# Optimization experiments

Hardware: AMD Instinct MI355X
Metric: run time of the kernel (lower is better)

The kernel has to match this reference:

```python
import jax, jax.numpy as jnp
import numpy as np

IN_DIM = 256
OUT_DIM = 64   # per-head dim
NUM_HEADS = 8
B = 8
N = 1024


def setup_inputs() -> dict:
    key = jax.random.key(0)
    k_adj, k_h, kq, kk, kv, kbq, kbk, kbv = jax.random.split(key, 8)
    adj_matrix = jax.random.randint(k_adj, (N, N), 0, 2, dtype=jnp.int32)
    h = jax.random.normal(k_h, (B, N, IN_DIM), dtype=jnp.float32)
    s = 1.0 / np.sqrt(IN_DIM)
    Wq = jax.random.normal(kq, (IN_DIM, OUT_DIM * NUM_HEADS), dtype=jnp.float32) * s
    Wk = jax.random.normal(kk, (IN_DIM, OUT_DIM * NUM_HEADS), dtype=jnp.float32) * s
    Wv = jax.random.normal(kv, (IN_DIM, OUT_DIM * NUM_HEADS), dtype=jnp.float32) * s
    bq = jax.random.normal(kbq, (OUT_DIM * NUM_HEADS,), dtype=jnp.float32) * 0.01
    bk = jax.random.normal(kbk, (OUT_DIM * NUM_HEADS,), dtype=jnp.float32) * 0.01
    bv = jax.random.normal(kbv, (OUT_DIM * NUM_HEADS,), dtype=jnp.float32) * 0.01
    return {"adj_matrix": adj_matrix, "h": h, "Wq": Wq, "bq": bq,
            "Wk": Wk, "bk": bk, "Wv": Wv, "bv": bv}


def reference(adj_matrix, h, Wq, bq, Wk, bk, Wv, bv):
    B_, N_, _ = h.shape
    H, D = NUM_HEADS, OUT_DIM
    Qh = (h @ Wq + bq).reshape(B_, N_, H, D)
    Kh = (h @ Wk + bk).reshape(B_, N_, H, D)
    Vh = (h @ Wv + bv).reshape(B_, N_, H, D)
    scores = jnp.einsum('bnhd,bmhd->bhnm', Qh, Kh) / jnp.sqrt(jnp.float32(D))
    # adjacency mask broadcast over batch and heads (neigh_attention=True)
    scores = jnp.where(adj_matrix[None, None, :, :] == 0, -jnp.inf, scores)
    attn = jax.nn.softmax(scores, axis=-1)
    out = jnp.einsum('bhnm,bmhd->bnhd', attn, Vh)
    return out.reshape(B_, N_, H * D)
```

## Files before the change

kernel.cpp:

```cpp
#include <hip/hip_runtime.h>
#include <hip/hip_bf16.h>
#include <math.h>

#define IN_DIM 256
#define HD     512
#define NHEADS 8
#define DH     64
#define NSEQ   1024
#define BATCH  8

#define QSCALE 0.18033688011112042f

typedef unsigned short u16;
typedef unsigned int   u32;
typedef short bf16x8 __attribute__((ext_vector_type(8)));
typedef float f32x4  __attribute__((ext_vector_type(4)));

#if __has_builtin(__builtin_amdgcn_exp2f)
#define EXP2(x) __builtin_amdgcn_exp2f(x)
#else
#define EXP2(x) __expf(0.69314718056f * (x))
#endif

static __device__ __forceinline__ u16 f2bf(float x) {
    u32 u = __builtin_bit_cast(u32, x);
    u += 0x7FFFu + ((u >> 16) & 1u);
    return (u16)(u >> 16);
}
static __device__ __forceinline__ float bf2f(u16 x) {
    return __builtin_bit_cast(float, ((u32)x) << 16);
}
static __device__ __forceinline__ u32 pk(u16 a, u16 b) {
    return (u32)a | ((u32)b << 16);
}
static __device__ __forceinline__ u32 cvtpk(float a, float b) {
    __hip_bfloat162 t = __float22bfloat162_rn(make_float2(a, b));
    u32 r; __builtin_memcpy(&r, &t, 4);
    return r;
}

__global__ __launch_bounds__(256)
void wtrans_kernel(const float* __restrict__ Wq, const float* __restrict__ Wk,
                   const float* __restrict__ Wv, u16* __restrict__ Wt)
{
    __shared__ float tile[64 * 65];
    const int bid = blockIdx.x, tid = threadIdx.x;
    const int k0 = (bid & 3) * 64, n0 = ((bid >> 2) & 7) * 64, wsel = bid >> 5;
    const float* W = (wsel == 0) ? Wq : (wsel == 1) ? Wk : Wv;
    u16* Out = Wt + (size_t)wsel * HD * IN_DIM;

    const int r = tid >> 2, c0 = (tid & 3) * 16;
#pragma unroll
    for (int j = 0; j < 16; j += 4) {
        float4 v = *(const float4*)(W + (size_t)(k0 + r) * HD + n0 + c0 + j);
        tile[r * 65 + c0 + j + 0] = v.x; tile[r * 65 + c0 + j + 1] = v.y;
        tile[r * 65 + c0 + j + 2] = v.z; tile[r * 65 + c0 + j + 3] = v.w;
    }
    __syncthreads();
    const int n = tid >> 2, ks = (tid & 3) * 16;
    u16 o[16];
#pragma unroll
    for (int j = 0; j < 16; ++j) o[j] = f2bf(tile[(ks + j) * 65 + n]);
    uint4 u0, u1;
    u0.x = pk(o[0], o[1]);   u0.y = pk(o[2], o[3]);
    u0.z = pk(o[4], o[5]);   u0.w = pk(o[6], o[7]);
    u1.x = pk(o[8], o[9]);   u1.y = pk(o[10], o[11]);
    u1.z = pk(o[12], o[13]); u1.w = pk(o[14], o[15]);
    u16* dst = Out + (size_t)(n0 + n) * IN_DIM + k0 + ks;
    *(uint4*)(dst) = u0;
    *(uint4*)(dst + 8) = u1;
}

__global__ __launch_bounds__(256, 4)
void gemm_mask_kernel(const float* __restrict__ h, const u16* __restrict__ Wt,
                      const int* __restrict__ adj,
                      const float* __restrict__ bq, const float* __restrict__ bk,
                      const float* __restrict__ bv,
                      u16* __restrict__ Qg, u16* __restrict__ Kg,
                      u16* __restrict__ Vtg, u16* __restrict__ MaddT)
{
    __shared__ u16 pool[64 * 64 + 3 * 64 * 64];
    const int tid = threadIdx.x;

    if (blockIdx.y >= 8) {
        int* tile = (int*)pool;
        const int abid = (blockIdx.y - 8) * 128 + blockIdx.x;
        const int tR = abid >> 4, tC = abid & 15;
        const int r = tid >> 2, cg = (tid & 3) * 16;
        const int* src = adj + (size_t)(tR * 64 + r) * NSEQ + tC * 64 + cg;
#pragma unroll
        for (int j = 0; j < 16; j += 4) {
            int4 a = *(const int4*)(src + j);
            tile[r * 65 + cg + j + 0] = a.x; tile[r * 65 + cg + j + 1] = a.y;
            tile[r * 65 + cg + j + 2] = a.z; tile[r * 65 + cg + j + 3] = a.w;
        }
        __syncthreads();
        const int kk = tid >> 2, qg = (tid & 3) * 16;
        u16 o[16];
#pragma unroll
        for (int j = 0; j < 16; ++j)
            o[j] = (tile[(qg + j) * 65 + kk] == 0) ? (u16)0xFF7F : (u16)0;
        uint4 u0, u1;
        u0.x = pk(o[0], o[1]);   u0.y = pk(o[2], o[3]);
        u0.z = pk(o[4], o[5]);   u0.w = pk(o[6], o[7]);
        u1.x = pk(o[8], o[9]);   u1.y = pk(o[10], o[11]);
        u1.z = pk(o[12], o[13]); u1.w = pk(o[14], o[15]);
        u16* dst = MaddT + (size_t)(tC * 64 + kk) * NSEQ + tR * 64 + qg;
        *(uint4*)(dst) = u0;
        *(uint4*)(dst + 8) = u1;
        return;
    }

    u16* As = pool;
    u16* Bs = pool + 64 * 64;

    const int m0 = blockIdx.x * 64;
    const int hh = blockIdx.y;
    const int n0 = hh * 64;

    const int w = tid >> 6, lane = tid & 63, l15 = lane & 15, quad = lane >> 4;
    const int sw = l15 & 7;

    f32x4 acc[3][4];
#pragma unroll
    for (int wh = 0; wh < 3; ++wh)
#pragma unroll
        for (int t = 0; t < 4; ++t) acc[wh][t] = (f32x4){0.f, 0.f, 0.f, 0.f};

    const int arow = tid >> 2, acg = (tid & 3) * 2;
    const int brow = tid & 63, bgrp = tid >> 6;
    const float* srcA = h + (size_t)(m0 + arow) * IN_DIM;

    for (int kk = 0; kk < IN_DIM; kk += 64) {
        __syncthreads();
#pragma unroll
        for (int g = 0; g < 2; ++g) {
            const float* p = srcA + kk + (acg + g) * 8;
            float4 v0 = *(const float4*)(p);
            float4 v1 = *(const float4*)(p + 4);
            uint4 u;
            u.x = cvtpk(v0.x, v0.y); u.y = cvtpk(v0.z, v0.w);
            u.z = cvtpk(v1.x, v1.y); u.w = cvtpk(v1.z, v1.w);
            *(uint4*)&As[arow * 64 + (((acg + g) ^ (arow & 7)) * 8)] = u;
        }
#pragma unroll
        for (int i = 0; i < 6; ++i) {
            const int gc = bgrp * 6 + i;
            const int wh = gc >> 3, c8 = gc & 7;
            *(uint4*)&Bs[wh * 4096 + brow * 64 + ((c8 ^ (brow & 7)) * 8)] =
                *(const uint4*)(Wt + (size_t)wh * HD * IN_DIM +
                                (size_t)(n0 + brow) * IN_DIM + kk + c8 * 8);
        }
        __syncthreads();
        const int ra = (w * 16 + l15) * 64;
        bf16x8 a0 = *(const bf16x8*)&As[ra + ((quad ^ sw) * 8)];
        bf16x8 a1 = *(const bf16x8*)&As[ra + (((4 + quad) ^ sw) * 8)];
#pragma unroll
        for (int t = 0; t < 4; ++t) {
            const int rb = (t * 16 + l15) * 64;
#pragma unroll
            for (int wh = 0; wh < 3; ++wh) {
                bf16x8 b0 = *(const bf16x8*)&Bs[wh * 4096 + rb + ((quad ^ sw) * 8)];
                bf16x8 b1 = *(const bf16x8*)&Bs[wh * 4096 + rb + (((4 + quad) ^ sw) * 8)];
                acc[wh][t] = __builtin_amdgcn_mfma_f32_16x16x32_bf16(a0, b0, acc[wh][t], 0, 0, 0);
                acc[wh][t] = __builtin_amdgcn_mfma_f32_16x16x32_bf16(a1, b1, acc[wh][t], 0, 0, 0);
            }
        }
    }

    for (int which = 0; which < 2; ++which) {
        u16* T = pool;
        const float* bias = (which == 0) ? bq : bk;
        u16* Out = (which == 0) ? Qg : Kg;
        const float scale = (which == 0) ? QSCALE : 1.0f;
        __syncthreads();
#pragma unroll
        for (int t = 0; t < 4; ++t) {
            const float bvv = bias[n0 + t * 16 + l15];
            const int rowb = w * 16 + quad * 4;
#pragma unroll
            for (int r = 0; r < 4; ++r)
                T[(rowb + r) * 72 + t * 16 + l15] =
                    f2bf((acc[which][t][r] + bvv) * scale);
        }
        __syncthreads();
        const int row = tid >> 2, qc = (tid & 3) * 16;
        u16* dst = Out + (size_t)(m0 + row) * HD + n0 + qc;
        const u16* srcT = &T[row * 72 + qc];
        *(uint4*)(dst)     = *(const uint4*)(srcT);
        *(uint4*)(dst + 8) = *(const uint4*)(srcT + 8);
    }

    {
        u16* T = pool;
        __syncthreads();
#pragma unroll
        for (int t = 0; t < 4; ++t) {
            const float bvv = bv[n0 + t * 16 + l15];
            const int trow = (t * 16 + l15) * 72;
#pragma unroll
            for (int r = 0; r < 4; ++r)
                T[trow + (quad * 4 + r) * 4 + w] = f2bf(acc[2][t][r] + bvv);
        }
        __syncthreads();
        const int b = m0 >> 10, nloc = m0 & 1023;
        const int d = tid >> 2, c = (tid & 3) * 16;
        u16* dst = Vtg + ((size_t)(b * NHEADS + hh) * DH + d) * NSEQ + nloc + c;
        *(uint4*)(dst)     = *(uint4*)&T[d * 72 + c];
        *(uint4*)(dst + 8) = *(uint4*)&T[d * 72 + c + 8];
    }
}

__global__ __launch_bounds__(256, 4)
void attn_kernel(const u16* __restrict__ MaddT, const u16* __restrict__ Qg,
                 const u16* __restrict__ Kg, const u16* __restrict__ Vtg,
                 float* __restrict__ out)
{
    __shared__ u16 Ks[2][64 * 64];
    __shared__ u16 Vs[2][64 * 64];
    __shared__ u16 Ps[64 * 64];

    const int tid = threadIdx.x;
    const int w = tid >> 6, lane = tid & 63, l15 = lane & 15, quad = lane >> 4;
    const int bh = blockIdx.x, qt = blockIdx.y;
    const int b = bh >> 3;
    const int n0 = qt * 64;
    const size_t rowbase = (size_t)b * NSEQ;
    const int colbase = (bh & 7) * DH;
    const int sw = l15 & 7;

    const u16* qrow = Qg + (rowbase + n0 + w * 16 + l15) * HD + colbase;
    const bf16x8 qa0 = *(const bf16x8*)(qrow + quad * 8);
    const bf16x8 qa1 = *(const bf16x8*)(qrow + 32 + quad * 8);

    const int srow = tid >> 2, cp = (tid & 3) * 2;
    const int swc0 = ((cp ^ (srow & 7)) * 8), swc1 = (((cp + 1) ^ (srow & 7)) * 8);
    const u16* kgp = Kg + (rowbase + srow) * HD + colbase + cp * 8;
    const u16* vgp = Vtg + ((size_t)bh * DH + srow) * NSEQ + cp * 8;
    const u16* mgp = MaddT + (size_t)l15 * NSEQ + n0 + w * 16 + quad * 4;

    uint4 kG0 = *(const uint4*)kgp, kG1 = *(const uint4*)(kgp + 8);
    uint4 vG0 = *(const uint4*)vgp, vG1 = *(const uint4*)(vgp + 8);
    ushort4 mG[4];
#pragma unroll
    for (int t = 0; t < 4; ++t) mG[t] = *(const ushort4*)(mgp + (size_t)(t * 16) * NSEQ);

    *(uint4*)&Ks[0][srow * 64 + swc0] = kG0;
    *(uint4*)&Ks[0][srow * 64 + swc1] = kG1;
    *(uint4*)&Vs[0][srow * 64 + swc0] = vG0;
    *(uint4*)&Vs[0][srow * 64 + swc1] = vG1;
    __syncthreads();

    float lrow[4] = {0.f, 0.f, 0.f, 0.f};
    f32x4 O[4];
#pragma unroll
    for (int t = 0; t < 4; ++t) O[t] = (f32x4){0.f, 0.f, 0.f, 0.f};

    const int pwbase = (w * 16 + quad * 4) * 64;
    const int parow  = (w * 16 + l15) * 64;

    for (int ch = 0; ch < 16; ++ch) {
        const int cur = ch & 1;

        f32x4 s4[4];
#pragma unroll
        for (int t = 0; t < 4; ++t)
            s4[t] = (f32x4){bf2f(mG[t].x), bf2f(mG[t].y),
                            bf2f(mG[t].z), bf2f(mG[t].w)};

        if (ch < 15) {
            kG0 = *(const uint4*)(kgp + (size_t)(ch + 1) * 64 * HD);
            kG1 = *(const uint4*)(kgp + (size_t)(ch + 1) * 64 * HD + 8);
            vG0 = *(const uint4*)(vgp + (ch + 1) * 64);
            vG1 = *(const uint4*)(vgp + (ch + 1) * 64 + 8);
#pragma unroll
            for (int t = 0; t < 4; ++t)
                mG[t] = *(const ushort4*)(mgp + ((size_t)(ch + 1) * 64 + t * 16) * NSEQ);
        }

#pragma unroll
        for (int t = 0; t < 4; ++t) {
            const int rb = (t * 16 + l15) * 64;
            bf16x8 kb0 = *(const bf16x8*)&Ks[cur][rb + ((quad ^ sw) * 8)];
            bf16x8 kb1 = *(const bf16x8*)&Ks[cur][rb + (((4 + quad) ^ sw) * 8)];
            s4[t] = __builtin_amdgcn_mfma_f32_16x16x32_bf16(qa0, kb0, s4[t], 0, 0, 0);
            s4[t] = __builtin_amdgcn_mfma_f32_16x16x32_bf16(qa1, kb1, s4[t], 0, 0, 0);
        }

        if (ch < 15) {
            *(uint4*)&Ks[1 - cur][srow * 64 + swc0] = kG0;
            *(uint4*)&Ks[1 - cur][srow * 64 + swc1] = kG1;
            *(uint4*)&Vs[1 - cur][srow * 64 + swc0] = vG0;
            *(uint4*)&Vs[1 - cur][srow * 64 + swc1] = vG1;
        }

#pragma unroll
        for (int r = 0; r < 4; ++r) {
            float p0 = EXP2(s4[0][r]);
            float p1 = EXP2(s4[1][r]);
            float p2 = EXP2(s4[2][r]);
            float p3 = EXP2(s4[3][r]);
            lrow[r] += (p0 + p1) + (p2 + p3);
            uint2 pw;
            pw.x = cvtpk(p0, p1);
            pw.y = cvtpk(p2, p3);
            const int q7 = (quad * 4 + r) & 7;
            *(uint2*)&Ps[pwbase + r * 64 + (((l15 >> 1) ^ q7) * 8) + (l15 & 1) * 4] = pw;
        }

        {
            bf16x8 pa0 = *(const bf16x8*)&Ps[parow + ((quad ^ sw) * 8)];
            bf16x8 pa1 = *(const bf16x8*)&Ps[parow + (((4 + quad) ^ sw) * 8)];
#pragma unroll
            for (int t = 0; t < 4; ++t) {
                const int rb = (t * 16 + l15) * 64;
                bf16x8 vb0 = *(const bf16x8*)&Vs[cur][rb + ((quad ^ sw) * 8)];
                bf16x8 vb1 = *(const bf16x8*)&Vs[cur][rb + (((4 + quad) ^ sw) * 8)];
                O[t] = __builtin_amdgcn_mfma_f32_16x16x32_bf16(pa0, vb0, O[t], 0, 0, 0);
                O[t] = __builtin_amdgcn_mfma_f32_16x16x32_bf16(pa1, vb1, O[t], 0, 0, 0);
            }
        }
        __syncthreads();
    }

#pragma unroll
    for (int d = 1; d < 16; d <<= 1)
#pragma unroll
        for (int r = 0; r < 4; ++r)
            lrow[r] += __shfl_xor(lrow[r], d, 64);

    float inv[4];
#pragma unroll
    for (int r = 0; r < 4; ++r) inv[r] = 1.0f / lrow[r];
#pragma unroll
    for (int t = 0; t < 4; ++t)
#pragma unroll
        for (int r = 0; r < 4; ++r)
            out[(rowbase + n0 + w * 16 + quad * 4 + r) * HD + colbase + t * 16 + l15] =
                O[t][r] * inv[r];
}

extern "C" void kernel_launch(void* const* d_in, const int* in_sizes, int n_in,
                              void* d_out, int out_size, void* d_ws, size_t ws_size,
                              hipStream_t stream) {
    const int*   adj = (const int*)d_in[0];
    const float* h   = (const float*)d_in[1];
    const float* Wq  = (const float*)d_in[2];
    const float* bq  = (const float*)d_in[3];
    const float* Wk  = (const float*)d_in[4];
    const float* bk  = (const float*)d_in[5];
    const float* Wv  = (const float*)d_in[6];
    const float* bv  = (const float*)d_in[7];
    float* outp = (float*)d_out;

    u16* Wt    = (u16*)d_ws;
    u16* Qg    = Wt + (size_t)3 * HD * IN_DIM;
    u16* Kg    = Qg + (size_t)BATCH * NSEQ * HD;
    u16* Vtg   = Kg + (size_t)BATCH * NSEQ * HD;
    u16* MaddT = Vtg + (size_t)BATCH * NSEQ * HD;

    wtrans_kernel<<<96, 256, 0, stream>>>(Wq, Wk, Wv, Wt);
    gemm_mask_kernel<<<dim3(BATCH * NSEQ / 64, 10), 256, 0, stream>>>(
        h, Wt, adj, bq, bk, bv, Qg, Kg, Vtg, MaddT);
    attn_kernel<<<dim3(BATCH * NHEADS, NSEQ / 64), 256, 0, stream>>>(
        MaddT, Qg, Kg, Vtg, outp);
}
```

Measured before the change: 143.4 us.

## Enlarge attention query tile to 128 rows with 512-thread blocks

Doubles the attention block to 8 waves handling 128 query rows, so each K/V chunk staged in shared memory is reused by twice as many query rows. Each thread now loads a single 16-byte K and V vector per chunk instead of two, and the P scratch buffer is doubled. This halves the number of blocks and raises the per-block shared-memory and thread footprint, which may reduce occupancy or wave-level parallelism across the GPU.

```diff
diff --git a/kernel.cpp b/kernel.cpp
--- a/kernel.cpp
+++ b/kernel.cpp
@@ -211,20 +211,20 @@
     }
 }
 
-__global__ __launch_bounds__(256, 4)
+__global__ __launch_bounds__(512, 4)
 void attn_kernel(const u16* __restrict__ MaddT, const u16* __restrict__ Qg,
                  const u16* __restrict__ Kg, const u16* __restrict__ Vtg,
                  float* __restrict__ out)
 {
     __shared__ u16 Ks[2][64 * 64];
     __shared__ u16 Vs[2][64 * 64];
-    __shared__ u16 Ps[64 * 64];
+    __shared__ u16 Ps[128 * 64];
 
     const int tid = threadIdx.x;
     const int w = tid >> 6, lane = tid & 63, l15 = lane & 15, quad = lane >> 4;
     const int bh = blockIdx.x, qt = blockIdx.y;
     const int b = bh >> 3;
-    const int n0 = qt * 64;
+    const int n0 = qt * 128;
     const size_t rowbase = (size_t)b * NSEQ;
     const int colbase = (bh & 7) * DH;
     const int sw = l15 & 7;
@@ -233,22 +233,20 @@
     const bf16x8 qa0 = *(const bf16x8*)(qrow + quad * 8);
     const bf16x8 qa1 = *(const bf16x8*)(qrow + 32 + quad * 8);
 
-    const int srow = tid >> 2, cp = (tid & 3) * 2;
-    const int swc0 = ((cp ^ (srow & 7)) * 8), swc1 = (((cp + 1) ^ (srow & 7)) * 8);
-    const u16* kgp = Kg + (rowbase + srow) * HD + colbase + cp * 8;
-    const u16* vgp = Vtg + ((size_t)bh * DH + srow) * NSEQ + cp * 8;
+    const int srow = tid >> 3, c8w = tid & 7;
+    const int swc = ((c8w ^ (srow & 7)) * 8);
+    const u16* kgp = Kg + (rowbase + srow) * HD + colbase + c8w * 8;
+    const u16* vgp = Vtg + ((size_t)bh * DH + srow) * NSEQ + c8w * 8;
     const u16* mgp = MaddT + (size_t)l15 * NSEQ + n0 + w * 16 + quad * 4;
 
-    uint4 kG0 = *(const uint4*)kgp, kG1 = *(const uint4*)(kgp + 8);
-    uint4 vG0 = *(const uint4*)vgp, vG1 = *(const uint4*)(vgp + 8);
+    uint4 kG = *(const uint4*)kgp;
+    uint4 vG = *(const uint4*)vgp;
     ushort4 mG[4];
 #pragma unroll
     for (int t = 0; t < 4; ++t) mG[t] = *(const ushort4*)(mgp + (size_t)(t * 16) * NSEQ);
 
-    *(uint4*)&Ks[0][srow * 64 + swc0] = kG0;
-    *(uint4*)&Ks[0][srow * 64 + swc1] = kG1;
-    *(uint4*)&Vs[0][srow * 64 + swc0] = vG0;
-    *(uint4*)&Vs[0][srow * 64 + swc1] = vG1;
+    *(uint4*)&Ks[0][srow * 64 + swc] = kG;
+    *(uint4*)&Vs[0][srow * 64 + swc] = vG;
     __syncthreads();
 
     float lrow[4] = {0.f, 0.f, 0.f, 0.f};
@@ -269,10 +267,8 @@
                             bf2f(mG[t].z), bf2f(mG[t].w)};
 
         if (ch < 15) {
-            kG0 = *(const uint4*)(kgp + (size_t)(ch + 1) * 64 * HD);
-            kG1 = *(const uint4*)(kgp + (size_t)(ch + 1) * 64 * HD + 8);
-            vG0 = *(const uint4*)(vgp + (ch + 1) * 64);
-            vG1 = *(const uint4*)(vgp + (ch + 1) * 64 + 8);
+            kG = *(const uint4*)(kgp + (size_t)(ch + 1) * 64 * HD);
+            vG = *(const uint4*)(vgp + (ch + 1) * 64);
 #pragma unroll
             for (int t = 0; t < 4; ++t)
                 mG[t] = *(const ushort4*)(mgp + ((size_t)(ch + 1) * 64 + t * 16) * NSEQ);
@@ -288,10 +284,8 @@
         }
 
         if (ch < 15) {
-            *(uint4*)&Ks[1 - cur][srow * 64 + swc0] = kG0;
-            *(uint4*)&Ks[1 - cur][srow * 64 + swc1] = kG1;
-            *(uint4*)&Vs[1 - cur][srow * 64 + swc0] = vG0;
-            *(uint4*)&Vs[1 - cur][srow * 64 + swc1] = vG1;
+            *(uint4*)&Ks[1 - cur][srow * 64 + swc] = kG;
+            *(uint4*)&Vs[1 - cur][srow * 64 + swc] = vG;
         }
 
 #pragma unroll
@@ -362,6 +356,6 @@
     wtrans_kernel<<<96, 256, 0, stream>>>(Wq, Wk, Wv, Wt);
     gemm_mask_kernel<<<dim3(BATCH * NSEQ / 64, 10), 256, 0, stream>>>(
         h, Wt, adj, bq, bk, bv, Qg, Kg, Vtg, MaddT);
-    attn_kernel<<<dim3(BATCH * NHEADS, NSEQ / 64), 256, 0, stream>>>(
+    attn_kernel<<<dim3(BATCH * NHEADS, NSEQ / 128), 512, 0, stream>>>(
         MaddT, Qg, Kg, Vtg, outp);
 }
```

After: 139.7 us. 1.03x faster.

## Switch attention to 32x32x16 MFMA with 128-row query tiles and permuted mask layout

Applied to the files above, without the earlier changes.

The attention kernel moves from 16x16x32 to 32x32x16 bf16 MFMA tiles. It computes S^T = K·Q^T so each lane owns one query row, and each block now covers 128 query rows. The mask-generation pass and the V transpose store are re-permuted so the additive mask and V columns match the 32x32 accumulator layout, and rows are read with 16-byte vector loads. Row sums reduce with a single shuffle and outputs are written as float4. The cost is that occupancy is halved (launch bounds 2), the grid shrinks to 512 blocks, and register pressure rises.

```diff
diff --git a/kernel.cpp b/kernel.cpp
--- a/kernel.cpp
+++ b/kernel.cpp
@@ -15,6 +15,7 @@
 typedef unsigned int   u32;
 typedef short bf16x8 __attribute__((ext_vector_type(8)));
 typedef float f32x4  __attribute__((ext_vector_type(4)));
+typedef float f32x16 __attribute__((ext_vector_type(16)));
 
 #if __has_builtin(__builtin_amdgcn_exp2f)
 #define EXP2(x) __builtin_amdgcn_exp2f(x)
@@ -27,9 +28,6 @@
     u += 0x7FFFu + ((u >> 16) & 1u);
     return (u16)(u >> 16);
 }
-static __device__ __forceinline__ float bf2f(u16 x) {
-    return __builtin_bit_cast(float, ((u32)x) << 16);
-}
 static __device__ __forceinline__ u32 pk(u16 a, u16 b) {
     return (u32)a | ((u32)b << 16);
 }
@@ -37,6 +35,16 @@
     __hip_bfloat162 t = __float22bfloat162_rn(make_float2(a, b));
     u32 r; __builtin_memcpy(&r, &t, 4);
     return r;
+}
+static __device__ __forceinline__ f32x16 maskinit(uint4 a, uint4 b) {
+    f32x16 c;
+    u32 ws[8] = {a.x, a.y, a.z, a.w, b.x, b.y, b.z, b.w};
+#pragma unroll
+    for (int i = 0; i < 8; ++i) {
+        c[2 * i]     = __builtin_bit_cast(float, ws[i] << 16);
+        c[2 * i + 1] = __builtin_bit_cast(float, ws[i] & 0xFFFF0000u);
+    }
+    return c;
 }
 
 __global__ __launch_bounds__(256)
@@ -77,7 +85,7 @@
                       const float* __restrict__ bq, const float* __restrict__ bk,
                       const float* __restrict__ bv,
                       u16* __restrict__ Qg, u16* __restrict__ Kg,
-                      u16* __restrict__ Vtg, u16* __restrict__ MaddT)
+                      u16* __restrict__ Vtg, u16* __restrict__ Madd2)
 {
     __shared__ u16 pool[64 * 64 + 3 * 64 * 64];
     const int tid = threadIdx.x;
@@ -95,17 +103,20 @@
             tile[r * 65 + cg + j + 2] = a.z; tile[r * 65 + cg + j + 3] = a.w;
         }
         __syncthreads();
-        const int kk = tid >> 2, qg = (tid & 3) * 16;
+        const int q = tid >> 2, p0 = (tid & 3) * 16;
         u16 o[16];
 #pragma unroll
-        for (int j = 0; j < 16; ++j)
-            o[j] = (tile[(qg + j) * 65 + kk] == 0) ? (u16)0xFF7F : (u16)0;
+        for (int j = 0; j < 16; ++j) {
+            const int p = p0 + j;
+            const int c = 32 * (p >> 5) + (p & 3) + 4 * ((p >> 4) & 1) + 8 * ((p >> 2) & 3);
+            o[j] = (tile[q * 65 + c] == 0) ? (u16)0xFF7F : (u16)0;
+        }
         uint4 u0, u1;
         u0.x = pk(o[0], o[1]);   u0.y = pk(o[2], o[3]);
         u0.z = pk(o[4], o[5]);   u0.w = pk(o[6], o[7]);
         u1.x = pk(o[8], o[9]);   u1.y = pk(o[10], o[11]);
         u1.z = pk(o[12], o[13]); u1.w = pk(o[14], o[15]);
-        u16* dst = MaddT + (size_t)(tC * 64 + kk) * NSEQ + tR * 64 + qg;
+        u16* dst = Madd2 + (size_t)(tR * 64 + q) * NSEQ + tC * 64 + p0;
         *(uint4*)(dst) = u0;
         *(uint4*)(dst + 8) = u1;
         return;
@@ -194,13 +205,16 @@
     {
         u16* T = pool;
         __syncthreads();
+        const int cb = 32 * (w >> 1) + 16 * (quad & 1) + 8 * (w & 1) + 4 * (quad >> 1);
 #pragma unroll
         for (int t = 0; t < 4; ++t) {
             const float bvv = bv[n0 + t * 16 + l15];
-            const int trow = (t * 16 + l15) * 72;
-#pragma unroll
-            for (int r = 0; r < 4; ++r)
-                T[trow + (quad * 4 + r) * 4 + w] = f2bf(acc[2][t][r] + bvv);
+            ushort4 o;
+            o.x = f2bf(acc[2][t][0] + bvv);
+            o.y = f2bf(acc[2][t][1] + bvv);
+            o.z = f2bf(acc[2][t][2] + bvv);
+            o.w = f2bf(acc[2][t][3] + bvv);
+            *(ushort4*)&T[(t * 16 + l15) * 72 + cb] = o;
         }
         __syncthreads();
         const int b = m0 >> 10, nloc = m0 & 1023;
@@ -211,39 +225,44 @@
     }
 }
 
-__global__ __launch_bounds__(256, 4)
-void attn_kernel(const u16* __restrict__ MaddT, const u16* __restrict__ Qg,
+__global__ __launch_bounds__(256, 2)
+void attn_kernel(const u16* __restrict__ Madd2, const u16* __restrict__ Qg,
                  const u16* __restrict__ Kg, const u16* __restrict__ Vtg,
                  float* __restrict__ out)
 {
     __shared__ u16 Ks[2][64 * 64];
     __shared__ u16 Vs[2][64 * 64];
-    __shared__ u16 Ps[64 * 64];
+    __shared__ u16 Ps[128 * 64];
 
     const int tid = threadIdx.x;
-    const int w = tid >> 6, lane = tid & 63, l15 = lane & 15, quad = lane >> 4;
+    const int w = tid >> 6, lane = tid & 63;
+    const int l31 = lane & 31, half = lane >> 5;
     const int bh = blockIdx.x, qt = blockIdx.y;
     const int b = bh >> 3;
-    const int n0 = qt * 64;
+    const int n0 = qt * 128;
     const size_t rowbase = (size_t)b * NSEQ;
     const int colbase = (bh & 7) * DH;
-    const int sw = l15 & 7;
-
-    const u16* qrow = Qg + (rowbase + n0 + w * 16 + l15) * HD + colbase;
-    const bf16x8 qa0 = *(const bf16x8*)(qrow + quad * 8);
-    const bf16x8 qa1 = *(const bf16x8*)(qrow + 32 + quad * 8);
+    const int q7 = l31 & 7;
+    const int qrow = w * 32 + l31;
+
+    const u16* qg = Qg + (rowbase + n0 + qrow) * HD + colbase;
+    bf16x8 qb[4];
+#pragma unroll
+    for (int s = 0; s < 4; ++s)
+        qb[s] = *(const bf16x8*)(qg + s * 16 + half * 8);
 
     const int srow = tid >> 2, cp = (tid & 3) * 2;
     const int swc0 = ((cp ^ (srow & 7)) * 8), swc1 = (((cp + 1) ^ (srow & 7)) * 8);
     const u16* kgp = Kg + (rowbase + srow) * HD + colbase + cp * 8;
     const u16* vgp = Vtg + ((size_t)bh * DH + srow) * NSEQ + cp * 8;
-    const u16* mgp = MaddT + (size_t)l15 * NSEQ + n0 + w * 16 + quad * 4;
+    const u16* mrow = Madd2 + (size_t)(n0 + qrow) * NSEQ + half * 16;
 
     uint4 kG0 = *(const uint4*)kgp, kG1 = *(const uint4*)(kgp + 8);
     uint4 vG0 = *(const uint4*)vgp, vG1 = *(const uint4*)(vgp + 8);
-    ushort4 mG[4];
-#pragma unroll
-    for (int t = 0; t < 4; ++t) mG[t] = *(const ushort4*)(mgp + (size_t)(t * 16) * NSEQ);
+    uint4 mA0 = *(const uint4*)(mrow);
+    uint4 mB0 = *(const uint4*)(mrow + 8);
+    uint4 mA1 = *(const uint4*)(mrow + 32);
+    uint4 mB1 = *(const uint4*)(mrow + 40);
 
     *(uint4*)&Ks[0][srow * 64 + swc0] = kG0;
     *(uint4*)&Ks[0][srow * 64 + swc1] = kG1;
@@ -251,40 +270,34 @@
     *(uint4*)&Vs[0][srow * 64 + swc1] = vG1;
     __syncthreads();
 
-    float lrow[4] = {0.f, 0.f, 0.f, 0.f};
-    f32x4 O[4];
-#pragma unroll
-    for (int t = 0; t < 4; ++t) O[t] = (f32x4){0.f, 0.f, 0.f, 0.f};
-
-    const int pwbase = (w * 16 + quad * 4) * 64;
-    const int parow  = (w * 16 + l15) * 64;
+    float lrow = 0.f;
+    f32x16 O0 = {}, O1 = {};
 
     for (int ch = 0; ch < 16; ++ch) {
         const int cur = ch & 1;
 
-        f32x4 s4[4];
-#pragma unroll
-        for (int t = 0; t < 4; ++t)
-            s4[t] = (f32x4){bf2f(mG[t].x), bf2f(mG[t].y),
-                            bf2f(mG[t].z), bf2f(mG[t].w)};
+        f32x16 st0 = maskinit(mA0, mB0);
+        f32x16 st1 = maskinit(mA1, mB1);
 
         if (ch < 15) {
             kG0 = *(const uint4*)(kgp + (size_t)(ch + 1) * 64 * HD);
             kG1 = *(const uint4*)(kgp + (size_t)(ch + 1) * 64 * HD + 8);
             vG0 = *(const uint4*)(vgp + (ch + 1) * 64);
             vG1 = *(const uint4*)(vgp + (ch + 1) * 64 + 8);
-#pragma unroll
-            for (int t = 0; t < 4; ++t)
-                mG[t] = *(const ushort4*)(mgp + ((size_t)(ch + 1) * 64 + t * 16) * NSEQ);
-        }
-
-#pragma unroll
-        for (int t = 0; t < 4; ++t) {
-            const int rb = (t * 16 + l15) * 64;
-            bf16x8 kb0 = *(const bf16x8*)&Ks[cur][rb + ((quad ^ sw) * 8)];
-            bf16x8 kb1 = *(const bf16x8*)&Ks[cur][rb + (((4 + quad) ^ sw) * 8)];
-            s4[t] = __builtin_amdgcn_mfma_f32_16x16x32_bf16(qa0, kb0, s4[t], 0, 0, 0);
-            s4[t] = __builtin_amdgcn_mfma_f32_16x16x32_bf16(qa1, kb1, s4[t], 0, 0, 0);
+            const u16* mnext = mrow + (ch + 1) * 64;
+            mA0 = *(const uint4*)(mnext);
+            mB0 = *(const uint4*)(mnext + 8);
+            mA1 = *(const uint4*)(mnext + 32);
+            mB1 = *(const uint4*)(mnext + 40);
+        }
+
+#pragma unroll
+        for (int s = 0; s < 4; ++s) {
+            const int g = ((s * 2 + half) ^ q7) * 8;
+            bf16x8 ka0 = *(const bf16x8*)&Ks[cur][l31 * 64 + g];
+            bf16x8 ka1 = *(const bf16x8*)&Ks[cur][(32 + l31) * 64 + g];
+            st0 = __builtin_amdgcn_mfma_f32_32x32x16_bf16(ka0, qb[s], st0, 0, 0, 0);
+            st1 = __builtin_amdgcn_mfma_f32_32x32x16_bf16(ka1, qb[s], st1, 0, 0, 0);
         }
 
         if (ch < 15) {
@@ -295,49 +308,52 @@
         }
 
 #pragma unroll
-        for (int r = 0; r < 4; ++r) {
-            float p0 = EXP2(s4[0][r]);
-            float p1 = EXP2(s4[1][r]);
-            float p2 = EXP2(s4[2][r]);
-            float p3 = EXP2(s4[3][r]);
-            lrow[r] += (p0 + p1) + (p2 + p3);
-            uint2 pw;
-            pw.x = cvtpk(p0, p1);
-            pw.y = cvtpk(p2, p3);
-            const int q7 = (quad * 4 + r) & 7;
-            *(uint2*)&Ps[pwbase + r * 64 + (((l15 >> 1) ^ q7) * 8) + (l15 & 1) * 4] = pw;
-        }
-
-        {
-            bf16x8 pa0 = *(const bf16x8*)&Ps[parow + ((quad ^ sw) * 8)];
-            bf16x8 pa1 = *(const bf16x8*)&Ps[parow + (((4 + quad) ^ sw) * 8)];
-#pragma unroll
-            for (int t = 0; t < 4; ++t) {
-                const int rb = (t * 16 + l15) * 64;
-                bf16x8 vb0 = *(const bf16x8*)&Vs[cur][rb + ((quad ^ sw) * 8)];
-                bf16x8 vb1 = *(const bf16x8*)&Vs[cur][rb + (((4 + quad) ^ sw) * 8)];
-                O[t] = __builtin_amdgcn_mfma_f32_16x16x32_bf16(pa0, vb0, O[t], 0, 0, 0);
-                O[t] = __builtin_amdgcn_mfma_f32_16x16x32_bf16(pa1, vb1, O[t], 0, 0, 0);
-            }
-        }
-        __syncthreads();
-    }
-
-#pragma unroll
-    for (int d = 1; d < 16; d <<= 1)
-#pragma unroll
-        for (int r = 0; r < 4; ++r)
-            lrow[r] += __shfl_xor(lrow[r], d, 64);
-
-    float inv[4];
-#pragma unroll
-    for (int r = 0; r < 4; ++r) inv[r] = 1.0f / lrow[r];
-#pragma unroll
-    for (int t = 0; t < 4; ++t)
-#pragma unroll
-        for (int r = 0; r < 4; ++r)
-            out[(rowbase + n0 + w * 16 + quad * 4 + r) * HD + colbase + t * 16 + l15] =
-                O[t][r] * inv[r];
+        for (int tile = 0; tile < 2; ++tile) {
+            const f32x16 st = tile ? st1 : st0;
+            float p[16];
+#pragma unroll
+            for (int r = 0; r < 16; ++r) p[r] = EXP2(st[r]);
+            float ps = 0.f;
+#pragma unroll
+            for (int r = 0; r < 16; ++r) ps += p[r];
+            lrow += ps;
+            uint4 w0, w1;
+            w0.x = cvtpk(p[0], p[1]);   w0.y = cvtpk(p[2], p[3]);
+            w0.z = cvtpk(p[4], p[5]);   w0.w = cvtpk(p[6], p[7]);
+            w1.x = cvtpk(p[8], p[9]);   w1.y = cvtpk(p[10], p[11]);
+            w1.z = cvtpk(p[12], p[13]); w1.w = cvtpk(p[14], p[15]);
+            const int g = tile * 4 + half * 2;
+            *(uint4*)&Ps[qrow * 64 + ((g ^ q7) * 8)]       = w0;
+            *(uint4*)&Ps[qrow * 64 + (((g + 1) ^ q7) * 8)] = w1;
+        }
+
+#pragma unroll
+        for (int s = 0; s < 4; ++s) {
+            const int g = ((s * 2 + half) ^ q7) * 8;
+            bf16x8 pb = *(const bf16x8*)&Ps[qrow * 64 + g];
+            bf16x8 va0 = *(const bf16x8*)&Vs[cur][l31 * 64 + g];
+            bf16x8 va1 = *(const bf16x8*)&Vs[cur][(32 + l31) * 64 + g];
+            O0 = __builtin_amdgcn_mfma_f32_32x32x16_bf16(va0, pb, O0, 0, 0, 0);
+            O1 = __builtin_amdgcn_mfma_f32_32x32x16_bf16(va1, pb, O1, 0, 0, 0);
+        }
+        __syncthreads();
+    }
+
+    lrow += __shfl_xor(lrow, 32, 64);
+    const float inv = 1.0f / lrow;
+
+    float* orow = out + (rowbase + n0 + qrow) * HD + colbase;
+#pragma unroll
+    for (int g = 0; g < 4; ++g) {
+        const int d0 = 4 * half + 8 * g;
+        float4 o0, o1;
+        o0.x = O0[4 * g + 0] * inv; o0.y = O0[4 * g + 1] * inv;
+        o0.z = O0[4 * g + 2] * inv; o0.w = O0[4 * g + 3] * inv;
+        o1.x = O1[4 * g + 0] * inv; o1.y = O1[4 * g + 1] * inv;
+        o1.z = O1[4 * g + 2] * inv; o1.w = O1[4 * g + 3] * inv;
+        *(float4*)(orow + d0)      = o0;
+        *(float4*)(orow + 32 + d0) = o1;
+    }
 }
 
 extern "C" void kernel_launch(void* const* d_in, const int* in_sizes, int n_in,
@@ -357,11 +373,11 @@
     u16* Qg    = Wt + (size_t)3 * HD * IN_DIM;
     u16* Kg    = Qg + (size_t)BATCH * NSEQ * HD;
     u16* Vtg   = Kg + (size_t)BATCH * NSEQ * HD;
-    u16* MaddT = Vtg + (size_t)BATCH * NSEQ * HD;
+    u16* Madd2 = Vtg + (size_t)BATCH * NSEQ * HD;
 
     wtrans_kernel<<<96, 256, 0, stream>>>(Wq, Wk, Wv, Wt);
     gemm_mask_kernel<<<dim3(BATCH * NSEQ / 64, 10), 256, 0, stream>>>(
-        h, Wt, adj, bq, bk, bv, Qg, Kg, Vtg, MaddT);
-    attn_kernel<<<dim3(BATCH * NHEADS, NSEQ / 64), 256, 0, stream>>>(
-        MaddT, Qg, Kg, Vtg, outp);
-}
+        h, Wt, adj, bq, bk, bv, Qg, Kg, Vtg, Madd2);
+    attn_kernel<<<dim3(BATCH * NHEADS, NSEQ / 128), 256, 0, stream>>>(
+        Madd2, Qg, Kg, Vtg, outp);
+}
```

New measurement: 131.5 us. -8.3%, faster.
